# Kernel optimization log

Measured on AMD Instinct MI355X. Metric: run time of the kernel, lower is better.

Reference implementation:

```python
import jax, jax.numpy as jnp
import numpy as np

B, H, W, C = 8, 64, 64, 768
NH, HD = 12, 64          # heads, head_dim
WS = 14                  # window size
MLP = 3072
EPS = 1e-6
SCALE = HD ** -0.5


def _layernorm(x, g, b):
    mu = jnp.mean(x, -1, keepdims=True)
    var = jnp.mean(jnp.square(x - mu), -1, keepdims=True)
    return (x - mu) * jax.lax.rsqrt(var + EPS) * g + b


def setup_inputs() -> dict:
    key = jax.random.key(0)
    ks = jax.random.split(key, 16)
    s = 0.02
    return {
        "hidden_states": jax.random.normal(ks[0], (B, H, W, C), jnp.float32),
        "ln1_g": jnp.ones((C,), jnp.float32),
        "ln1_b": jnp.zeros((C,), jnp.float32),
        "qkv_w": jax.random.normal(ks[1], (C, 3 * C), jnp.float32) * s,  # (in, out)
        "qkv_b": jnp.zeros((3 * C,), jnp.float32),
        "proj_w": jax.random.normal(ks[2], (C, C), jnp.float32) * s,
        "proj_b": jnp.zeros((C,), jnp.float32),
        "rel_pos_h": jax.random.normal(ks[3], (2 * WS - 1, HD), jnp.float32) * s,
        "rel_pos_w": jax.random.normal(ks[4], (2 * WS - 1, HD), jnp.float32) * s,
        "ln2_g": jnp.ones((C,), jnp.float32),
        "ln2_b": jnp.zeros((C,), jnp.float32),
        "lin1_w": jax.random.normal(ks[5], (C, MLP), jnp.float32) * s,
        "lin1_b": jnp.zeros((MLP,), jnp.float32),
        "lin2_w": jax.random.normal(ks[6], (MLP, C), jnp.float32) * s,
        "lin2_b": jnp.zeros((C,), jnp.float32),
    }


def _attention(x, qkv_w, qkv_b, proj_w, proj_b, rel_pos_h, rel_pos_w):
    # x: (Bw, WS, WS, C) windows
    Bw = x.shape[0]
    N = WS * WS
    qkv = (x.reshape(Bw, N, C) @ qkv_w + qkv_b)              # (Bw, N, 3C)
    qkv = qkv.reshape(Bw, N, 3, NH, HD).transpose(2, 0, 3, 1, 4)
    qkv = qkv.reshape(3, Bw * NH, N, HD)
    q, k, v = qkv[0], qkv[1], qkv[2]
    attn = jnp.einsum('bqd,bkd->bqk', q * SCALE, k)          # (Bw*NH, N, N)
    # decomposed relative position bias (q_size == k_size == WS, no interpolation)
    coords = jnp.arange(WS)[:, None] - jnp.arange(WS)[None, :] + (WS - 1)  # (WS, WS)
    Rh = rel_pos_h[coords]                                    # (WS, WS, HD)
    Rw = rel_pos_w[coords]
    r_q = q.reshape(Bw * NH, WS, WS, HD)
    rel_h = jnp.einsum('bhwc,hkc->bhwk', r_q, Rh)
    rel_w = jnp.einsum('bhwc,wkc->bhwk', r_q, Rw)
    attn = attn.reshape(Bw * NH, WS, WS, WS, WS)
    attn = attn + rel_h[:, :, :, :, None] + rel_w[:, :, :, None, :]
    attn = attn.reshape(Bw * NH, N, N)
    attn = jax.nn.softmax(attn.astype(jnp.float32), axis=-1).astype(q.dtype)
    out = jnp.einsum('bqk,bkd->bqd', attn, v)                 # (Bw*NH, N, HD)
    out = out.reshape(Bw, NH, WS, WS, HD).transpose(0, 2, 3, 1, 4).reshape(Bw, WS, WS, C)
    return out @ proj_w + proj_b


def _layer(x, p):
    residual = x
    h = _layernorm(x, p['ln1_g'], p['ln1_b'])
    # window partition with padding 64 -> 70
    pad_h = (WS - H % WS) % WS
    pad_w = (WS - W % WS) % WS
    h = jnp.pad(h, ((0, 0), (0, pad_h), (0, pad_w), (0, 0)))
    Hp, Wp = H + pad_h, W + pad_w
    nh, nw = Hp // WS, Wp // WS
    h = h.reshape(B, nh, WS, nw, WS, C).transpose(0, 1, 3, 2, 4, 5).reshape(-1, WS, WS, C)
    h = _attention(h, p['qkv_w'], p['qkv_b'], p['proj_w'], p['proj_b'],
                   p['rel_pos_h'], p['rel_pos_w'])
    # unpartition + crop
    h = h.reshape(B, nh, nw, WS, WS, C).transpose(0, 1, 3, 2, 4, 5).reshape(B, Hp, Wp, C)
    h = h[:, :H, :W, :]
    h = residual + h
    ln2 = _layernorm(h, p['ln2_g'], p['ln2_b'])
    mlp = jax.nn.gelu(ln2 @ p['lin1_w'] + p['lin1_b'], approximate=False) @ p['lin2_w'] + p['lin2_b']
    return h + mlp


def reference(hidden_states, ln1_g, ln1_b, qkv_w, qkv_b, proj_w, proj_b,
              rel_pos_h, rel_pos_w, ln2_g, ln2_b, lin1_w, lin1_b, lin2_w, lin2_b):
    p = dict(ln1_g=ln1_g, ln1_b=ln1_b, qkv_w=qkv_w, qkv_b=qkv_b,
             proj_w=proj_w, proj_b=proj_b, rel_pos_h=rel_pos_h, rel_pos_w=rel_pos_w,
             ln2_g=ln2_g, ln2_b=ln2_b, lin1_w=lin1_w, lin1_b=lin1_b,
             lin2_w=lin2_w, lin2_b=lin2_b)
    return _layer(hidden_states, p)
```

## Files before the change

kernel.cpp:

```cpp
#include <hip/hip_runtime.h>
#include <hip/hip_bf16.h>
#include <math.h>
#include <stdint.h>

typedef unsigned short u16;
typedef __attribute__((ext_vector_type(8))) short bf16x8;
typedef __attribute__((ext_vector_type(4))) float f32x4;

__device__ __forceinline__ float b2f(u16 u) {
  union { float f; uint32_t i; } v; v.i = ((uint32_t)u) << 16; return v.f;
}
__device__ __forceinline__ u16 f2b(float f) {
  union { float f; uint32_t i; } v; v.f = f;
  uint32_t x = v.i;
  return (u16)((x + 0x7fffu + ((x >> 16) & 1u)) >> 16);
}

__device__ __forceinline__ void gl_lds16(const u16* g, u16* l) {
  __builtin_amdgcn_global_load_lds(
      (const __attribute__((address_space(1))) void*)g,
      (__attribute__((address_space(3))) void*)l, 16, 0, 0);
}

__global__ __launch_bounds__(256)
void transpose_w(const float* __restrict__ in, u16* __restrict__ out, int K, int N) {
  __shared__ float t[32][33];
  const int x = threadIdx.x & 31;
  const int y = threadIdx.x >> 5;
  const int n0 = blockIdx.x * 32;
  const int k0 = blockIdx.y * 32;
  #pragma unroll
  for (int yy = 0; yy < 32; yy += 8)
    t[y + yy][x] = in[(size_t)(k0 + y + yy) * N + n0 + x];
  __syncthreads();
  #pragma unroll
  for (int yy = 0; yy < 32; yy += 8)
    out[(size_t)(n0 + y + yy) * K + k0 + x] = f2b(t[x][y + yy]);
}

__global__ __launch_bounds__(256)
void rel_cast(const float* __restrict__ rph, const float* __restrict__ rpw,
              u16* __restrict__ RHB, u16* __restrict__ RWB)
{
  const int i = blockIdx.x * 256 + threadIdx.x;
  if (i < 27 * 64) { RHB[i] = f2b(rph[i]); RWB[i] = f2b(rpw[i]); }
}

__global__ __launch_bounds__(256)
void ln_f32(const float* __restrict__ xin, const float* __restrict__ g,
            const float* __restrict__ b, u16* __restrict__ out)
{
  const int R = blockIdx.x * 4 + (threadIdx.x >> 6);
  const int lane = threadIdx.x & 63;
  const float* p = xin + (size_t)R * 768 + lane * 12;
  float v[12];
  float4 a0 = *(const float4*)(p);
  float4 a1 = *(const float4*)(p + 4);
  float4 a2 = *(const float4*)(p + 8);
  v[0]=a0.x; v[1]=a0.y; v[2]=a0.z;  v[3]=a0.w;
  v[4]=a1.x; v[5]=a1.y; v[6]=a1.z;  v[7]=a1.w;
  v[8]=a2.x; v[9]=a2.y; v[10]=a2.z; v[11]=a2.w;
  float sum = 0.f, sq = 0.f;
  #pragma unroll
  for (int i = 0; i < 12; ++i) { sum += v[i]; sq += v[i] * v[i]; }
  #pragma unroll
  for (int m = 1; m < 64; m <<= 1) { sum += __shfl_xor(sum, m); sq += __shfl_xor(sq, m); }
  const float mu  = sum * (1.0f / 768.0f);
  const float var = sq * (1.0f / 768.0f) - mu * mu;
  const float rs  = rsqrtf(var + 1e-6f);
  u16 o[12];
  #pragma unroll
  for (int i = 0; i < 12; ++i)
    o[i] = f2b((v[i] - mu) * rs * g[lane * 12 + i] + b[lane * 12 + i]);
  u16* q = out + (size_t)R * 768 + lane * 12;
  *(ushort4*)(q)     = make_ushort4(o[0], o[1], o[2],  o[3]);
  *(ushort4*)(q + 4) = make_ushort4(o[4], o[5], o[6],  o[7]);
  *(ushort4*)(q + 8) = make_ushort4(o[8], o[9], o[10], o[11]);
}

__global__ __launch_bounds__(256)
void qkv_padfill(const float* __restrict__ qkv_b,
                 u16* __restrict__ Qb, u16* __restrict__ Kb, u16* __restrict__ Vtb)
{
  const int R = blockIdx.x * 4 + (threadIdx.x >> 6);
  const int lane = threadIdx.x & 63;
  const int win = R / 196, n = R - win * 196;
  const int r25 = win % 25;
  const int wh = r25 / 5, ww = r25 - wh * 5;
  const int ii = n / 14,  jj = n - ii * 14;
  const int gh = wh * 14 + ii, gw = ww * 14 + jj;
  if (gh < 64 && gw < 64) return;
  #pragma unroll
  for (int head = 0; head < 12; ++head) {
    const size_t bh = (size_t)(win * 12 + head);
    Qb[(bh * 196 + n) * 64 + lane]  = f2b(qkv_b[head * 64 + lane]);
    Kb[(bh * 196 + n) * 64 + lane]  = f2b(qkv_b[768 + head * 64 + lane] * 0.125f);
    Vtb[(bh * 64 + lane) * 224 + n] = f2b(qkv_b[1536 + head * 64 + lane]);
  }
}

template<int EPI>
__global__ __launch_bounds__(256)
void gemm_bt(const u16* __restrict__ A, const u16* __restrict__ BT,
             int M, int N, int K,
             const float* __restrict__ bias,
             void* __restrict__ out0, u16* __restrict__ out1, u16* __restrict__ out2,
             const float* __restrict__ extra)
{
  __shared__ __align__(16) u16 As[128 * 32];
  __shared__ __align__(16) u16 Bs[128 * 32];
  const int tid  = threadIdx.x;
  const int lane = tid & 63;
  const int wave = tid >> 6;

  const int nwg = gridDim.x * gridDim.y;
  const int lid = blockIdx.y * gridDim.x + blockIdx.x;
  const int nl  = (lid & 7) * (nwg >> 3) + (lid >> 3);
  const int bx  = nl / gridDim.y;
  const int by  = nl - bx * gridDim.y;
  const int m0 = bx * 128;
  const int n0 = by * 128;

  const int wm = (wave >> 1) << 6;
  const int wn = (wave & 1) << 6;
  const int cl = lane & 15;
  const int q4 = lane >> 4;

  f32x4 acc[4][4];
  #pragma unroll
  for (int i = 0; i < 4; ++i)
    #pragma unroll
    for (int j = 0; j < 4; ++j) acc[i][j] = f32x4{0.f, 0.f, 0.f, 0.f};

  const int sr = tid >> 2;
  const int sk = (tid & 3) << 3;
  const u16* ag0 = A  + (size_t)(m0 + sr) * K + sk;
  const u16* ag1 = A  + (size_t)(m0 + 64 + sr) * K + sk;
  const u16* bg0 = BT + (size_t)(n0 + sr) * K + sk;
  const u16* bg1 = BT + (size_t)(n0 + 64 + sr) * K + sk;

  for (int k0 = 0; k0 < K; k0 += 32) {
    __syncthreads();
    gl_lds16(ag0 + k0, &As[tid * 8]);
    gl_lds16(ag1 + k0, &As[tid * 8 + 2048]);
    gl_lds16(bg0 + k0, &Bs[tid * 8]);
    gl_lds16(bg1 + k0, &Bs[tid * 8 + 2048]);
    __syncthreads();
    bf16x8 af[4], bfv[4];
    #pragma unroll
    for (int i = 0; i < 4; ++i) af[i]  = *(const bf16x8*)&As[(wm + i * 16 + cl) * 32 + q4 * 8];
    #pragma unroll
    for (int i = 0; i < 4; ++i) bfv[i] = *(const bf16x8*)&Bs[(wn + i * 16 + cl) * 32 + q4 * 8];
    #pragma unroll
    for (int i = 0; i < 4; ++i)
      #pragma unroll
      for (int j = 0; j < 4; ++j)
        acc[i][j] = __builtin_amdgcn_mfma_f32_16x16x32_bf16(af[i], bfv[j], acc[i][j], 0, 0, 0);
  }

  #pragma unroll
  for (int mt = 0; mt < 4; ++mt) {
    int rowW[4], rowN[4];
    if (EPI == 0) {
      #pragma unroll
      for (int i = 0; i < 4; ++i) {
        const int grow = m0 + wm + mt * 16 + q4 * 4 + i;
        const int bb = grow >> 12, rem = grow & 4095;
        const int gh = rem >> 6, gw = rem & 63;
        const int wh = gh / 14, ii = gh - wh * 14;
        const int ww = gw / 14, jj = gw - ww * 14;
        rowW[i] = (bb * 25 + wh * 5 + ww) * 12;
        rowN[i] = ii * 14 + jj;
      }
    }
    #pragma unroll
    for (int nt = 0; nt < 4; ++nt) {
      const int gcol = n0 + wn + nt * 16 + cl;
      const float bval = bias[gcol];
      if (EPI == 0) {
        const int s = (gcol >= 1536) ? 2 : (gcol >= 768 ? 1 : 0);
        const int rem2 = gcol - s * 768;
        const int head = rem2 >> 6, hd = rem2 & 63;
        #pragma unroll
        for (int i = 0; i < 4; ++i) {
          const float v = acc[mt][nt][i] + bval;
          const size_t bh = (size_t)(rowW[i] + head);
          if (s == 0)      ((u16*)out0)[(bh * 196 + rowN[i]) * 64 + hd] = f2b(v);
          else if (s == 1) out1[(bh * 196 + rowN[i]) * 64 + hd] = f2b(v * 0.125f);
          else             out2[(bh * 64 + hd) * 224 + rowN[i]] = f2b(v);
        }
      } else if (EPI == 1) {
        #pragma unroll
        for (int i = 0; i < 4; ++i) {
          const int grow = m0 + wm + mt * 16 + q4 * 4 + i;
          const size_t idx = (size_t)grow * 768 + gcol;
          ((float*)out0)[idx] = acc[mt][nt][i] + bval + extra[idx];
        }
      } else {
        #pragma unroll
        for (int i = 0; i < 4; ++i) {
          const int grow = m0 + wm + mt * 16 + q4 * 4 + i;
          const float v = acc[mt][nt][i] + bval;
          const float u2 = v * (1.5957691216f + 0.0713548163f * v * v);
          const float gl = v / (1.0f + __expf(-u2));
          ((u16*)out0)[(size_t)grow * 3072 + gcol] = f2b(gl);
        }
      }
    }
  }
}

__global__ __launch_bounds__(256)
void attn_kernel(const u16* __restrict__ Qb, const u16* __restrict__ Kb,
                 const u16* __restrict__ Vtb,
                 const u16* __restrict__ RHB, const u16* __restrict__ RWB,
                 u16* __restrict__ outO)
{
  __shared__ __align__(16) float Ss[32 * 201];
  __shared__ u16 MhAll[196 * 14];
  __shared__ u16 MwAll[196 * 14];
  __shared__ float Sinv[32];
  u16* Ps = (u16*)Ss;

  const int tid  = threadIdx.x;
  const int lane = tid & 63;
  const int wave = tid >> 6;
  const int cl = lane & 15;
  const int q4 = lane >> 4;
  const int bh = blockIdx.x;
  const int win = bh / 12, head = bh - win * 12;
  const int bb = win / 25, r25 = win - bb * 25;
  const int wwh = r25 / 5, www = r25 - wwh * 5;

  const u16* Qbh = Qb  + (size_t)bh * 196 * 64;
  const u16* Kbh = Kb  + (size_t)bh * 196 * 64;
  const u16* Vbh = Vtb + (size_t)bh * 64 * 224;

  for (int t = wave; t < 28; t += 4) {
    const int isW = t >= 14;
    const int grp = isW ? t - 14 : t;
    const int qrow = isW ? cl * 14 + grp : grp * 14 + cl;
    int trow = grp - cl + 13; trow = trow < 0 ? 0 : trow;
    const u16* TB = isW ? RWB : RHB;
    f32x4 acc = f32x4{0.f, 0.f, 0.f, 0.f};
    #pragma unroll
    for (int ks = 0; ks < 2; ++ks) {
      bf16x8 a  = *(const bf16x8*)(Qbh + (size_t)qrow * 64 + ks * 32 + q4 * 8);
      bf16x8 bv = *(const bf16x8*)(TB + (size_t)trow * 64 + ks * 32 + q4 * 8);
      acc = __builtin_amdgcn_mfma_f32_16x16x32_bf16(a, bv, acc, 0, 0, 0);
    }
    if (cl < 14) {
      #pragma unroll
      for (int i = 0; i < 4; ++i) {
        const int r = q4 * 4 + i;
        if (r < 14) {
          if (isW) MwAll[(r * 14 + grp) * 14 + cl] = f2b(acc[i]);
          else     MhAll[(grp * 14 + r) * 14 + cl] = f2b(acc[i]);
        }
      }
    }
  }
  __syncthreads();

  for (int c = 0; c < 7; ++c) {
    const int qbase = c * 32;
    bf16x8 afr[2][2];
    #pragma unroll
    for (int mt = 0; mt < 2; ++mt)
      #pragma unroll
      for (int ks = 0; ks < 2; ++ks)
        afr[mt][ks] = *(const bf16x8*)(Qbh + (size_t)(qbase + mt * 16 + cl) * 64 + ks * 32 + q4 * 8);

    for (int t = wave; t < 26; t += 4) {
      const int mt = t / 13, nt = t - mt * 13;
      const int col = nt * 16 + cl;
      f32x4 acc = f32x4{0.f, 0.f, 0.f, 0.f};
      #pragma unroll
      for (int ks = 0; ks < 2; ++ks) {
        bf16x8 bv = *(const bf16x8*)(Kbh + (size_t)col * 64 + ks * 32 + q4 * 8);
        acc = __builtin_amdgcn_mfma_f32_16x16x32_bf16(afr[mt][ks], bv, acc, 0, 0, 0);
      }
      if (col < 196) {
        const int kh = col / 14, kw = col - kh * 14;
        #pragma unroll
        for (int i = 0; i < 4; ++i) {
          const int r = mt * 16 + q4 * 4 + i;
          const int gq = qbase + r;
          float bias = 0.f;
          if (gq < 196) bias = b2f(MhAll[gq * 14 + kh]) + b2f(MwAll[gq * 14 + kw]);
          Ss[r * 201 + col] = acc[i] + bias;
        }
      }
    }
    __syncthreads();

    const int r = wave * 8 + (lane >> 3);
    const int s = lane & 7;
    float e[25];
    float sum = 0.f;
    #pragma unroll
    for (int k = 0; k < 25; ++k) {
      const int col = s + 8 * k;
      float ex = 0.f;
      if (col < 196) ex = __expf(fminf(Ss[r * 201 + col], 60.f));
      e[k] = ex;
      sum += ex;
    }
    sum += __shfl_xor(sum, 1);
    sum += __shfl_xor(sum, 2);
    sum += __shfl_xor(sum, 4);
    if (s == 0) Sinv[r] = 1.0f / sum;
    __syncthreads();

    #pragma unroll
    for (int k = 0; k < 25; ++k) {
      const int col = s + 8 * k;
      Ps[r * 232 + col] = (col < 196) ? f2b(e[k]) : (u16)0;
    }
    for (int z = tid; z < 384; z += 256) {
      const int rr = z / 12, m = z - rr * 12;
      *(uint32_t*)&Ps[rr * 232 + 200 + 2 * m] = 0;
    }
    __syncthreads();

    {
      const int hd = wave * 16 + cl;
      f32x4 acc0 = f32x4{0.f, 0.f, 0.f, 0.f};
      f32x4 acc1 = f32x4{0.f, 0.f, 0.f, 0.f};
      #pragma unroll
      for (int ks = 0; ks < 7; ++ks) {
        bf16x8 bv = *(const bf16x8*)(Vbh + (size_t)hd * 224 + ks * 32 + q4 * 8);
        bf16x8 a0 = *(const bf16x8*)&Ps[(cl)      * 232 + ks * 32 + q4 * 8];
        bf16x8 a1 = *(const bf16x8*)&Ps[(16 + cl) * 232 + ks * 32 + q4 * 8];
        acc0 = __builtin_amdgcn_mfma_f32_16x16x32_bf16(a0, bv, acc0, 0, 0, 0);
        acc1 = __builtin_amdgcn_mfma_f32_16x16x32_bf16(a1, bv, acc1, 0, 0, 0);
      }
      #pragma unroll
      for (int i = 0; i < 4; ++i) {
        #pragma unroll
        for (int half = 0; half < 2; ++half) {
          const int q = qbase + half * 16 + q4 * 4 + i;
          if (q < 196) {
            const float av = (half ? acc1[i] : acc0[i]) * Sinv[half * 16 + q4 * 4 + i];
            const int ii = q / 14, jj = q - ii * 14;
            const int gh = wwh * 14 + ii, gw = www * 14 + jj;
            if (gh < 64 && gw < 64)
              outO[(((size_t)bb * 64 + gh) * 64 + gw) * 768 + head * 64 + hd] = f2b(av);
          }
        }
      }
    }
    __syncthreads();
  }
}

extern "C" void kernel_launch(void* const* d_in, const int* in_sizes, int n_in,
                              void* d_out, int out_size, void* d_ws, size_t ws_size,
                              hipStream_t stream)
{
  (void)in_sizes; (void)n_in; (void)out_size; (void)ws_size;
  const float* x      = (const float*)d_in[0];
  const float* ln1_g  = (const float*)d_in[1];
  const float* ln1_b  = (const float*)d_in[2];
  const float* qkv_w  = (const float*)d_in[3];
  const float* qkv_b  = (const float*)d_in[4];
  const float* proj_w = (const float*)d_in[5];
  const float* proj_b = (const float*)d_in[6];
  const float* rph    = (const float*)d_in[7];
  const float* rpw    = (const float*)d_in[8];
  const float* ln2_g  = (const float*)d_in[9];
  const float* ln2_b  = (const float*)d_in[10];
  const float* lin1_w = (const float*)d_in[11];
  const float* lin1_b = (const float*)d_in[12];
  const float* lin2_w = (const float*)d_in[13];
  const float* lin2_b = (const float*)d_in[14];
  float* outF = (float*)d_out;

  char* ws = (char*)d_ws;
  size_t off = 0;
  auto allocB = [&](size_t bytes) -> char* {
    char* p = ws + off;
    off += (bytes + 255) & ~(size_t)255;
    return p;
  };
  u16* qkvT  = (u16*)allocB((size_t)2304 * 768 * 2);
  u16* projT = (u16*)allocB((size_t)768 * 768 * 2);
  u16* lin1T = (u16*)allocB((size_t)3072 * 768 * 2);
  u16* lin2T = (u16*)allocB((size_t)768 * 3072 * 2);
  u16* RHB   = (u16*)allocB((size_t)(27 * 64 + 64) * 2);
  u16* RWB   = (u16*)allocB((size_t)(27 * 64 + 64) * 2);
  u16* xn    = (u16*)allocB((size_t)32768 * 768 * 2);
  char* region = allocB((size_t)201326592);
  u16* Qb   = (u16*)region;
  u16* Kb   = Qb + (size_t)30105600;
  u16* Vtb  = Kb + (size_t)30105600;
  float* hbuf = (float*)region;
  u16* midQ = (u16*)(region + (size_t)100663296);

  dim3 blk(256);
  transpose_w<<<dim3(72, 24), blk, 0, stream>>>(qkv_w,  qkvT, 768, 2304);
  transpose_w<<<dim3(24, 24), blk, 0, stream>>>(proj_w, projT, 768, 768);
  transpose_w<<<dim3(96, 24), blk, 0, stream>>>(lin1_w, lin1T, 768, 3072);
  transpose_w<<<dim3(24, 96), blk, 0, stream>>>(lin2_w, lin2T, 3072, 768);
  rel_cast<<<7, blk, 0, stream>>>(rph, rpw, RHB, RWB);

  ln_f32<<<8192, blk, 0, stream>>>(x, ln1_g, ln1_b, xn);

  gemm_bt<0><<<dim3(256, 18), blk, 0, stream>>>(xn, qkvT, 32768, 2304, 768,
                                                qkv_b, Qb, Kb, Vtb, nullptr);
  qkv_padfill<<<9800, blk, 0, stream>>>(qkv_b, Qb, Kb, Vtb);

  attn_kernel<<<2400, blk, 0, stream>>>(Qb, Kb, Vtb, RHB, RWB, xn);

  gemm_bt<1><<<dim3(256, 6), blk, 0, stream>>>(xn, projT, 32768, 768, 768,
                                               proj_b, hbuf, nullptr, nullptr, x);

  ln_f32<<<8192, blk, 0, stream>>>(hbuf, ln2_g, ln2_b, xn);

  for (int pass = 0; pass < 2; ++pass) {
    const size_t ro = (size_t)pass * 16384;
    gemm_bt<2><<<dim3(128, 24), blk, 0, stream>>>(xn + ro * 768, lin1T, 16384, 3072, 768,
                                                  lin1_b, midQ, nullptr, nullptr, nullptr);
    gemm_bt<1><<<dim3(128, 6), blk, 0, stream>>>(midQ, lin2T, 16384, 768, 3072,
                                                 lin2_b, outF + ro * 768, nullptr, nullptr,
                                                 hbuf + ro * 768);
  }
}
```

Before: 1.470 ms.

## Triple-buffer GEMM LDS tiles with async global-to-LDS prefetch two stages ahead

Replaces the single-buffered GEMM K loop, which synchronised before and after each tile load, with a three-buffer ring. The next two K tiles are prefetched via global_load_lds while the current one is computed, using an explicit vmcnt wait and one barrier per iteration. The residual read in the projection epilogue also becomes a nontemporal load. This raises LDS use per block, which may reduce occupancy.

```diff
diff --git a/kernel.cpp b/kernel.cpp
--- a/kernel.cpp
+++ b/kernel.cpp
@@ -107,8 +107,8 @@
              void* __restrict__ out0, u16* __restrict__ out1, u16* __restrict__ out2,
              const float* __restrict__ extra)
 {
-  __shared__ __align__(16) u16 As[128 * 32];
-  __shared__ __align__(16) u16 Bs[128 * 32];
+  __shared__ __align__(16) u16 As3[3 * 4096];
+  __shared__ __align__(16) u16 Bs3[3 * 4096];
   const int tid  = threadIdx.x;
   const int lane = tid & 63;
   const int wave = tid >> 6;
@@ -139,24 +139,50 @@
   const u16* bg0 = BT + (size_t)(n0 + sr) * K + sk;
   const u16* bg1 = BT + (size_t)(n0 + 64 + sr) * K + sk;
 
-  for (int k0 = 0; k0 < K; k0 += 32) {
-    __syncthreads();
-    gl_lds16(ag0 + k0, &As[tid * 8]);
-    gl_lds16(ag1 + k0, &As[tid * 8 + 2048]);
-    gl_lds16(bg0 + k0, &Bs[tid * 8]);
-    gl_lds16(bg1 + k0, &Bs[tid * 8 + 2048]);
-    __syncthreads();
+  const int nt = K >> 5;
+
+  auto STAGE = [&](int buf, int k0) {
+    u16* as = As3 + buf * 4096;
+    u16* bs = Bs3 + buf * 4096;
+    gl_lds16(ag0 + k0, &as[tid * 8]);
+    gl_lds16(ag1 + k0, &as[tid * 8 + 2048]);
+    gl_lds16(bg0 + k0, &bs[tid * 8]);
+    gl_lds16(bg1 + k0, &bs[tid * 8 + 2048]);
+  };
+  auto COMPUTE = [&](int buf) {
+    const u16* as = As3 + buf * 4096;
+    const u16* bs = Bs3 + buf * 4096;
     bf16x8 af[4], bfv[4];
     #pragma unroll
-    for (int i = 0; i < 4; ++i) af[i]  = *(const bf16x8*)&As[(wm + i * 16 + cl) * 32 + q4 * 8];
-    #pragma unroll
-    for (int i = 0; i < 4; ++i) bfv[i] = *(const bf16x8*)&Bs[(wn + i * 16 + cl) * 32 + q4 * 8];
+    for (int i = 0; i < 4; ++i) af[i]  = *(const bf16x8*)&as[(wm + i * 16 + cl) * 32 + q4 * 8];
+    #pragma unroll
+    for (int i = 0; i < 4; ++i) bfv[i] = *(const bf16x8*)&bs[(wn + i * 16 + cl) * 32 + q4 * 8];
     #pragma unroll
     for (int i = 0; i < 4; ++i)
       #pragma unroll
       for (int j = 0; j < 4; ++j)
         acc[i][j] = __builtin_amdgcn_mfma_f32_16x16x32_bf16(af[i], bfv[j], acc[i][j], 0, 0, 0);
-  }
+  };
+
+  STAGE(0, 0);
+  STAGE(1, 32);
+
+  int bufc = 0;
+  for (int t = 0; t < nt - 1; ++t) {
+    asm volatile("s_waitcnt vmcnt(4)" ::: "memory");
+    __builtin_amdgcn_s_barrier();
+    __builtin_amdgcn_sched_barrier(0);
+    if (t + 2 < nt) {
+      const int nb = (bufc + 2 >= 3) ? bufc - 1 : bufc + 2;
+      STAGE(nb, (t + 2) << 5);
+    }
+    COMPUTE(bufc);
+    bufc = (bufc + 1 == 3) ? 0 : bufc + 1;
+  }
+  asm volatile("s_waitcnt vmcnt(0)" ::: "memory");
+  __builtin_amdgcn_s_barrier();
+  __builtin_amdgcn_sched_barrier(0);
+  COMPUTE(bufc);
 
   #pragma unroll
   for (int mt = 0; mt < 4; ++mt) {
@@ -174,8 +200,8 @@
       }
     }
     #pragma unroll
-    for (int nt = 0; nt < 4; ++nt) {
-      const int gcol = n0 + wn + nt * 16 + cl;
+    for (int nt2 = 0; nt2 < 4; ++nt2) {
+      const int gcol = n0 + wn + nt2 * 16 + cl;
       const float bval = bias[gcol];
       if (EPI == 0) {
         const int s = (gcol >= 1536) ? 2 : (gcol >= 768 ? 1 : 0);
@@ -183,7 +209,7 @@
         const int head = rem2 >> 6, hd = rem2 & 63;
         #pragma unroll
         for (int i = 0; i < 4; ++i) {
-          const float v = acc[mt][nt][i] + bval;
+          const float v = acc[mt][nt2][i] + bval;
           const size_t bh = (size_t)(rowW[i] + head);
           if (s == 0)      ((u16*)out0)[(bh * 196 + rowN[i]) * 64 + hd] = f2b(v);
           else if (s == 1) out1[(bh * 196 + rowN[i]) * 64 + hd] = f2b(v * 0.125f);
@@ -194,13 +220,14 @@
         for (int i = 0; i < 4; ++i) {
           const int grow = m0 + wm + mt * 16 + q4 * 4 + i;
           const size_t idx = (size_t)grow * 768 + gcol;
-          ((float*)out0)[idx] = acc[mt][nt][i] + bval + extra[idx];
+          const float ex = __builtin_nontemporal_load(&extra[idx]);
+          ((float*)out0)[idx] = acc[mt][nt2][i] + bval + ex;
         }
       } else {
         #pragma unroll
         for (int i = 0; i < 4; ++i) {
           const int grow = m0 + wm + mt * 16 + q4 * 4 + i;
-          const float v = acc[mt][nt][i] + bval;
+          const float v = acc[mt][nt2][i] + bval;
           const float u2 = v * (1.5957691216f + 0.0713548163f * v * v);
           const float gl = v / (1.0f + __expf(-u2));
           ((u16*)out0)[(size_t)grow * 3072 + gcol] = f2b(gl);
```

Result: faster. 1.272 ms (-13.5%).
